# Performance work log

Hardware: AMD Instinct MI355X
Metric: run time of the kernel (lower is better)

## Reference

```python
import jax, jax.numpy as jnp
import numpy as np

K = 3        # kernel_size
EPS = 1e-4   # eps from __init__


def _conv_valid(x, w):
    # NHWC input, HWIO filter, VALID padding, stride 1
    return jax.lax.conv_general_dilated(
        x, w, window_strides=(1, 1), padding='VALID',
        dimension_numbers=('NHWC', 'HWIO', 'NHWC'))


def _backward_standardize_weight(grad_in, original_weights, gain, w_max_bitmap, eps):
    # Faithful translation of BackwardInjectWSConv2D.backward_standardize_weight
    kh, kw, cin, cout = original_weights.shape
    N = float(kh * kw * cin)                       # b*h*w in the TF code
    mu = jnp.mean(original_weights, axis=(0, 1, 2))
    xmu = original_weights - mu                    # [K,K,Cin,Cout]
    var = jnp.mean(jnp.square(xmu), axis=(0, 1, 2))
    mvar = N * var
    maxvar = jnp.maximum(mvar, eps)
    sqrtvar = jnp.sqrt(maxvar)
    ivar = 1.0 / sqrtvar
    givar = gain * ivar                            # [Cout]
    dgivar = jnp.sum(grad_in * xmu, axis=(0, 1, 2))
    divar = dgivar * gain
    dgain = dgivar * ivar
    dxmu1 = grad_in * givar
    dsqrtvar = (-1.0 / jnp.square(sqrtvar)) * divar
    dmaxvar = (0.5 / jnp.sqrt(maxvar)) * dsqrtvar
    dmvar = w_max_bitmap * dmaxvar
    dvar = N * dmvar
    dsq = (1.0 / N) * dvar                         # (1/N)*ones_like(grad_in)*dvar, broadcast
    dxmu2 = 2.0 * xmu * dsq
    dx1 = dxmu1 + dxmu2
    dmu = -jnp.sum(dx1, axis=(0, 1, 2))
    dx2 = (1.0 / N) * dmu                          # broadcast over [K,K,Cin]
    dx = dx1 + dx2
    return dx, dgain


def setup_inputs() -> dict:
    key = jax.random.key(0)
    ks = jax.random.split(key, 5)
    B, H, W, Cin, Cout = 64, 56, 56, 128, 128
    return {
        'grad_output': jax.random.normal(ks[0], (B, H, W, Cout), jnp.float32),
        'inputs': jax.random.normal(ks[1], (B, H, W, Cin), jnp.float32),
        'kernels': jax.random.normal(ks[2], (K, K, Cin, Cout), jnp.float32),
        'std_kernels': jax.random.normal(ks[3], (K, K, Cin, Cout), jnp.float32),
        'gain': jax.random.uniform(ks[4], (Cout,), jnp.float32),
        'w_max_bitmap': jnp.ones((Cout,), jnp.float32),
    }


def reference(grad_output, inputs, kernels, std_kernels, gain, w_max_bitmap):
    pad = (K - 1) // 2
    # ---- grad wrt input: full conv of grad_out with rot180(std_kernels), io swapped
    go_pad = jnp.pad(grad_output, ((0, 0), (pad, pad), (pad, pad), (0, 0)))
    w_rot = jnp.transpose(std_kernels[::-1, ::-1], (0, 1, 3, 2))   # [K,K,Cout,Cin]
    manual_grad_in = _conv_valid(go_pad, w_rot)                    # [B,H,W,Cin]
    # ---- grad wrt weight: treat Cin as batch, B as contraction channel
    in_pad = jnp.pad(inputs, ((0, 0), (pad, pad), (pad, pad), (0, 0)))
    fmt_inp = jnp.transpose(in_pad, (3, 1, 2, 0))                  # [Cin,H+2p,W+2p,B]
    fmt_wt = jnp.transpose(grad_output, (1, 2, 0, 3))              # [H,W,B,Cout]
    direct = _conv_valid(fmt_inp, fmt_wt)                          # [Cin,K,K,Cout]
    grad_wt_raw = jnp.transpose(direct, (1, 2, 0, 3))              # [K,K,Cin,Cout]
    # ---- weight-standardization backward chain
    manual_grad_wt, manual_grad_gain = _backward_standardize_weight(
        grad_wt_raw, kernels, gain, w_max_bitmap, EPS)
    # ---- bias grad
    manual_grad_bias = jnp.sum(grad_output, axis=(0, 1, 2))        # [Cout]
    return manual_grad_in, manual_grad_wt, manual_grad_bias, manual_grad_gain
```

## Files before the change

kernel.cpp:

```cpp
#include <hip/hip_runtime.h>
#include <hip/hip_bf16.h>

typedef __bf16 bf16x8 __attribute__((ext_vector_type(8)));
typedef __bf16 bf16x4 __attribute__((ext_vector_type(4)));
typedef float  f32x4  __attribute__((ext_vector_type(4)));
typedef unsigned int u32;

#define HW_   3136
#define NPIX  200704
#define GI_ELEMS 25690112

#define GOT_OFF   0u
#define RAW_OFF   51380224u
#define BIASA_OFF 51970048u
#define STDKF_OFF 51970560u
#define GUARD_OFF 52265472u
#define ZB_OFF    52265728u
#define ZA_OFF    52272000u
#define X_OFF     52279168u

__device__ __forceinline__ f32x4 mfma16(bf16x8 a, bf16x8 b, f32x4 c){
  return __builtin_amdgcn_mfma_f32_16x16x32_bf16(a, b, c, 0, 0, 0);
}

__device__ __forceinline__ void async16(const void* g, __bf16* l){
  __builtin_amdgcn_global_load_lds(
      (const __attribute__((address_space(1))) void*)g,
      (__attribute__((address_space(3))) void*)l, 16, 0, 0);
}

__global__ __launch_bounds__(256) void k_prep(const float* __restrict__ s, __bf16* __restrict__ d){
  const int g = blockIdx.x*256 + threadIdx.x;
  const int l = g & 63;
  const int j = (g >> 6) & 7;
  const int kc = (g >> 9) & 3;
  const int tap = g >> 11;
  const int ci = j*16 + (l & 15);
  const int co0 = kc*32 + (l >> 4)*8;
  const float* src = s + ((size_t)(tap*128 + ci))*128 + co0;
  f32x4 x0 = *(const f32x4*)src;
  f32x4 x1 = *(const f32x4*)(src + 4);
  bf16x8 y;
  #pragma unroll
  for (int e=0;e<4;e++){ y[e] = (__bf16)x0[e]; y[e+4] = (__bf16)x1[e]; }
  *(bf16x8*)(d + (size_t)g*8) = y;
}

__global__ __launch_bounds__(256) void k_goT(const float* __restrict__ go,
                                             __bf16* __restrict__ goT,
                                             __bf16* __restrict__ goB,
                                             float* __restrict__ biasA){
  __shared__ __bf16 T[64][130];
  __shared__ float biasS[128];
  const int t = threadIdx.x;
  const size_t p0 = (size_t)blockIdx.x*64;
  if (t < 128) biasS[t] = 0.f;
  __syncthreads();
  float bs[4] = {0.f,0.f,0.f,0.f};
  const int co0 = (t*4) & 127;
  #pragma unroll
  for (int i=0;i<8;i++){
    const int flat = (i*256+t)*4;
    const int px = flat >> 7, co = flat & 127;
    f32x4 x = *(const f32x4*)(go + p0*128 + flat);
    bf16x4 y;
    #pragma unroll
    for (int e=0;e<4;e++){ y[e] = (__bf16)x[e]; bs[e] += x[e]; }
    *(bf16x4*)&T[px][co] = y;
    *(bf16x4*)(goB + p0*128 + flat) = y;
  }
  #pragma unroll
  for (int e=0;e<4;e++) atomicAdd(&biasS[co0+e], bs[e]);
  __syncthreads();
  #pragma unroll
  for (int j=0;j<2;j++){
    const int task = j*256 + t;
    const int co = task >> 2, q = task & 3;
    bf16x8 v0, v1;
    #pragma unroll
    for (int k=0;k<8;k++) v0[k] = T[q*16+k][co];
    #pragma unroll
    for (int k=0;k<8;k++) v1[k] = T[q*16+8+k][co];
    __bf16* d = goT + (size_t)co*NPIX + p0 + q*16;
    *(bf16x8*)d = v0; *(bf16x8*)(d+8) = v1;
  }
  if (t < 128) atomicAdd(&biasA[t], biasS[t]);
}

__global__ __launch_bounds__(256) void k_inT(const float* __restrict__ inp,
                                             __bf16* __restrict__ inT){
  __shared__ __bf16 T[64][130];
  const int t = threadIdx.x;
  const size_t p0 = (size_t)blockIdx.x*64;

  if (blockIdx.x < 2304){
    const int g = blockIdx.x*256 + t;
    const int pair = g / 72, k = g - pair*72;
    __bf16* base = inT + (size_t)pair*3712;
    int off;
    if (k < 8)       off = k*8;
    else if (k < 16) off = 57*64 + (k-8)*8;
    else             off = (k-15)*64 + 56;
    bf16x8 z = {};
    *(bf16x8*)(base + off) = z;
  }

  #pragma unroll
  for (int i=0;i<8;i++){
    const int flat = (i*256+t)*4;
    const int px = flat >> 7, ci = flat & 127;
    f32x4 x = *(const f32x4*)(inp + p0*128 + flat);
    bf16x4 y;
    #pragma unroll
    for (int e=0;e<4;e++) y[e] = (__bf16)x[e];
    *(bf16x4*)&T[px][ci] = y;
  }
  __syncthreads();
  #pragma unroll
  for (int j=0;j<4;j++){
    const int task = j*256 + t;
    const int ci = task >> 3, ch = task & 7;
    const int p = (int)p0 + ch*8;
    const int b = p / HW_; const int r = p - b*HW_;
    const int h = r / 56;  const int w = r - h*56;
    bf16x8 v;
    #pragma unroll
    for (int k=0;k<8;k++) v[k] = T[ch*8+k][ci];
    *(bf16x8*)(inT + (((size_t)(ci*64+b))*58 + (h+1))*64 + w) = v;
  }
}

__global__ __launch_bounds__(256, 1) void k_gradin9(const __bf16* __restrict__ goB,
                                                    const __bf16* __restrict__ stdkF,
                                                    const __bf16* __restrict__ zsrc,
                                                    float* __restrict__ out){
  __shared__ char LDS[44544];
  const int t = threadIdx.x;
  const int wv = t >> 6, l = t & 63, lr = l & 15, lg = l >> 4;
  const int b = blockIdx.x, h0 = blockIdx.y*4;
  const int j0 = (wv & 1)*4;
  const int pxg = (wv >> 1)*112;

  int sb[7];
  #pragma unroll
  for (int tile=0; tile<7; ++tile){
    const int p = pxg + tile*16 + lr;
    const int ro = p / 56; const int w = p - ro*56;
    sb[tile] = (ro + 2)*58 + (w + 2);
  }

  f32x4 acc[7][4];
  #pragma unroll
  for (int i=0;i<7;i++){
    #pragma unroll
    for (int j=0;j<4;j++){
      #pragma unroll
      for (int r=0;r<4;r++) acc[i][j][r] = 0.f;
    }
  }

  for (int c=0; c<2; ++c){
    #pragma unroll
    for (int it=0; it<11; ++it){
      const int qb = it*256 + wv*64;
      const u32 q = (u32)(qb + l);
      if (q < 2784u){
        const u32 r = q / 464u;
        const u32 rem = q - r*464u;
        const u32 wp = rem >> 3;
        const u32 cl = rem & 7u;
        const int h = h0 - 1 + (int)r;
        const u32 s = r*58u + wp;
        const u32 csrc = cl ^ (s & 7u);
        const bool valid = (h >= 0) & (h < 56) & (wp >= 1u) & (wp <= 56u);
        const __bf16* src = valid
          ? goB + ((size_t)((b*HW_) + h*56 + ((int)wp - 1))*128 + c*64 + csrc*8)
          : zsrc;
        async16(src, (__bf16*)(LDS + qb*16));
      }
    }
    __syncthreads();

    for (int tap=0; tap<9; ++tap){
      const int u = tap/3;
      const int soff = u*58 + (tap - u*3);
      #pragma unroll
      for (int kc=0; kc<2; ++kc){
        const int kcg = c*2 + kc;
        bf16x8 Bf[4];
        #pragma unroll
        for (int j=0;j<4;++j)
          Bf[j] = *(const bf16x8*)(stdkF + ((size_t)(((tap*4 + kcg)*8 + j0 + j)*64 + l))*8);
        bf16x8 Af[7];
        #pragma unroll
        for (int tile=0;tile<7;++tile){
          const int s = sb[tile] - soff;
          const int byte = (s << 7) | (((kc*4 + lg) ^ (s & 7)) << 4);
          Af[tile] = *(const bf16x8*)(LDS + byte);
        }
        #pragma unroll
        for (int tile=0;tile<7;++tile){
          #pragma unroll
          for (int j=0;j<4;++j)
            acc[tile][j] = mfma16(Af[tile], Bf[j], acc[tile][j]);
        }
      }
    }
    __syncthreads();
  }

  float* o = out + ((size_t)b*HW_ + (size_t)h0*56 + pxg)*128;
  #pragma unroll
  for (int tile=0;tile<7;++tile){
    #pragma unroll
    for (int j=0;j<4;++j){
      #pragma unroll
      for (int r=0;r<4;++r)
        o[(size_t)(tile*16 + 4*lg + r)*128 + (j0 + j)*16 + lr] = acc[tile][j][r];
    }
  }
}

#define KSTEP9(ks)                                                             \
{                                                                              \
  const int pl = (ks)*32 + lg*8;                                               \
  const int q  = (ks)*4 + lg;                                                  \
  const int hl = q / 7;                                                        \
  const int w0 = pl - hl*56;                                                   \
  const int plc = ((ks)==3 && lg==3) ? 112 : pl;                               \
  bf16x8 b0 = *(const bf16x8*)&Bb[(wco + lr)*120 + plc];                       \
  bf16x8 b1 = *(const bf16x8*)&Bb[(wco + 16 + lr)*120 + plc];                  \
  const __bf16* abase = &Ab[lr*264 + hl*64 + w0];                              \
  _Pragma("unroll")                                                            \
  for (int u=0; u<3; ++u){                                                     \
    const __bf16* ap = abase + u*64;                                           \
    union { bf16x8 v; u32 d[4]; } vp, va, vn, a0, a2;                          \
    vp.v = *(const bf16x8*)(ap - 8);                                           \
    va.v = *(const bf16x8*)ap;                                                 \
    vn.v = *(const bf16x8*)(ap + 8);                                           \
    if ((ks)==3 && lg >= 2){                                                   \
      vp.d[0]=0u; vp.d[1]=0u; vp.d[2]=0u; vp.d[3]=0u;                          \
      va.d[0]=0u; va.d[1]=0u; va.d[2]=0u; va.d[3]=0u;                          \
      vn.d[0]=0u; vn.d[1]=0u; vn.d[2]=0u; vn.d[3]=0u;                          \
    }                                                                          \
    a0.d[0] = (va.d[0] << 16) | (vp.d[3] >> 16);                               \
    a0.d[1] = (va.d[1] << 16) | (va.d[0] >> 16);                               \
    a0.d[2] = (va.d[2] << 16) | (va.d[1] >> 16);                               \
    a0.d[3] = (va.d[3] << 16) | (va.d[2] >> 16);                               \
    a2.d[0] = (va.d[0] >> 16) | (va.d[1] << 16);                               \
    a2.d[1] = (va.d[1] >> 16) | (va.d[2] << 16);                               \
    a2.d[2] = (va.d[2] >> 16) | (va.d[3] << 16);                               \
    a2.d[3] = (va.d[3] >> 16) | (vn.d[0] << 16);                               \
    acc[u*3+0][0] = mfma16(a0.v, b0, acc[u*3+0][0]);                           \
    acc[u*3+0][1] = mfma16(a0.v, b1, acc[u*3+0][1]);                           \
    acc[u*3+1][0] = mfma16(va.v, b0, acc[u*3+1][0]);                           \
    acc[u*3+1][1] = mfma16(va.v, b1, acc[u*3+1][1]);                           \
    acc[u*3+2][0] = mfma16(a2.v, b0, acc[u*3+2][0]);                           \
    acc[u*3+2][1] = mfma16(a2.v, b1, acc[u*3+2][1]);                           \
  }                                                                            \
}

__global__ __launch_bounds__(256, 2) void k_gradwt9(const char* __restrict__ ws,
                                                    float* __restrict__ raw){
  __shared__ __bf16 LDS[39208];
  const int t = threadIdx.x;
  const int w = t >> 6, l = t & 63, lr = l & 15, lg = l >> 4;
  const int b = blockIdx.x, ci0 = blockIdx.y*16;
  const int wco = w*32;

  if (t < 40){
    const int idx = (t < 8) ? (30720 + t) : ((t < 24) ? (34952 + t - 8) : (39192 + t - 24));
    LDS[idx] = (__bf16)0.f;
  }

  u32 boff[8];
  #pragma unroll
  for (int i=0;i<8;i++){
    const int chunk = i*256 + t;
    if (chunk < 1920){
      const int co = chunk / 15, part = chunk - co*15;
      boff[i] = (part < 14)
        ? (GOT_OFF + (u32)(co*NPIX + b*HW_ + part*8)*2u)
        : ZB_OFF;
    } else boff[i] = ZB_OFF;
  }
  u32 aoff[3];
  #pragma unroll
  for (int i=0;i<3;i++){
    const int chunk = i*256 + t;
    if (chunk < 528){
      const int ci = chunk / 33, r = chunk - ci*33;
      aoff[i] = (r < 32)
        ? (X_OFF + (u32)((((ci0+ci)*64 + b)*58 + (r>>3))*64 + (r&7)*8)*2u)
        : ZA_OFF;
    } else aoff[i] = ZA_OFF;
  }

  f32x4 acc[9][2];
  #pragma unroll
  for (int tp=0;tp<9;tp++){
    #pragma unroll
    for (int j=0;j<2;j++){
      #pragma unroll
      for (int r=0;r<4;r++) acc[tp][j][r] = 0.f;
    }
  }

  #pragma unroll
  for (int i=0;i<8;i++){
    const int chunk = i*256 + t;
    if (chunk < 1920){ async16(ws + boff[i], LDS + chunk*8); boff[i] += 224u; }
  }
  #pragma unroll
  for (int i=0;i<3;i++){
    const int chunk = i*256 + t;
    if (chunk < 528){ async16(ws + aoff[i], LDS + 30728 + chunk*8); aoff[i] += 256u; }
  }
  __syncthreads();

  for (int c=0; c<28; ++c){
    const int cur = c & 1;
    if (c < 27){
      __bf16* dB = LDS + ((cur ^ 1) ? 15360 : 0);
      __bf16* dA = LDS + ((cur ^ 1) ? 34968 : 30728);
      #pragma unroll
      for (int i=0;i<8;i++){
        const int chunk = i*256 + t;
        if (chunk < 1920){ async16(ws + boff[i], dB + chunk*8); boff[i] += 224u; }
      }
      #pragma unroll
      for (int i=0;i<3;i++){
        const int chunk = i*256 + t;
        if (chunk < 528){ async16(ws + aoff[i], dA + chunk*8); aoff[i] += 256u; }
      }
    }
    const __bf16* Bb = LDS + (cur ? 15360 : 0);
    const __bf16* Ab = LDS + (cur ? 34968 : 30728);
    KSTEP9(0) KSTEP9(1) KSTEP9(2) KSTEP9(3)
    __syncthreads();
  }

  #pragma unroll
  for (int tp=0;tp<9;tp++){
    #pragma unroll
    for (int j=0;j<2;j++){
      #pragma unroll
      for (int r=0;r<4;r++)
        atomicAdd(&raw[(size_t)(tp*128 + ci0 + 4*lg + r)*128 + wco + j*16 + lr],
                  acc[tp][j][r]);
    }
  }
}

__global__ __launch_bounds__(128) void k_std(const float* __restrict__ raw,
      const float* __restrict__ kern, const float* __restrict__ gain,
      const float* __restrict__ bmap, const float* __restrict__ biasA,
      float* __restrict__ out_wt, float* __restrict__ out_bias, float* __restrict__ out_gain){
  const int co = blockIdx.x, t = threadIdx.x;
  float kv[9], gv[9];
  float s1=0.f, s2=0.f, sg=0.f, sgk=0.f;
  #pragma unroll
  for (int i=0;i<9;i++){
    const int m = t + i*128;
    const float k_ = kern[(size_t)m*128 + co];
    const float g_ = raw [(size_t)m*128 + co];
    kv[i]=k_; gv[i]=g_;
    s1 += k_; s2 += k_*k_; sg += g_; sgk += g_*k_;
  }
  __shared__ float red[4][128];
  red[0][t]=s1; red[1][t]=s2; red[2][t]=sg; red[3][t]=sgk;
  __syncthreads();
  for (int off=64; off>0; off>>=1){
    if (t < off){
      red[0][t]+=red[0][t+off]; red[1][t]+=red[1][t+off];
      red[2][t]+=red[2][t+off]; red[3][t]+=red[3][t+off];
    }
    __syncthreads();
  }
  const float N = 1152.f;
  const float S1=red[0][0], S2=red[1][0], Sg=red[2][0], Sgk=red[3][0];
  const float mu = S1/N;
  const float var = S2/N - mu*mu;
  const float mvar = N*var;
  const float maxvar = fmaxf(mvar, 1e-4f);
  const float sqrtvar = sqrtf(maxvar);
  const float ivar = 1.f/sqrtvar;
  const float g = gain[co];
  const float givar = g*ivar;
  const float dgivar = Sgk - mu*Sg;
  const float divar = dgivar*g;
  const float dsqrtvar = -divar/maxvar;
  const float dmaxvar = 0.5f*dsqrtvar/sqrtvar;
  const float dsq = bmap[co]*dmaxvar;
  const float dmu = -(givar*Sg + 2.f*dsq*(S1 - N*mu));
  const float dmuN = dmu*(1.f/N);
  #pragma unroll
  for (int i=0;i<9;i++){
    const int m = t + i*128;
    out_wt[(size_t)m*128 + co] = gv[i]*givar + 2.f*(kv[i]-mu)*dsq + dmuN;
  }
  if (t == 0){ out_gain[co] = dgivar*ivar; out_bias[co] = biasA[co]; }
}

extern "C" void kernel_launch(void* const* d_in, const int* in_sizes, int n_in,
                              void* d_out, int out_size, void* d_ws, size_t ws_size,
                              hipStream_t stream){
  const float* go   = (const float*)d_in[0];
  const float* inp  = (const float*)d_in[1];
  const float* kern = (const float*)d_in[2];
  const float* stdk = (const float*)d_in[3];
  const float* gain = (const float*)d_in[4];
  const float* bmap = (const float*)d_in[5];

  char* ws = (char*)d_ws;
  __bf16* goT   = (__bf16*)(ws + GOT_OFF);
  float*  raw   = (float*) (ws + RAW_OFF);
  float*  biasA = (float*) (ws + BIASA_OFF);
  __bf16* stdkF = (__bf16*)(ws + STDKF_OFF);
  char*   guard =           ws + GUARD_OFF;
  __bf16* goB   = (__bf16*)(ws + X_OFF);
  __bf16* inT   = (__bf16*)(ws + X_OFF);

  hipMemsetAsync(ws + RAW_OFF,   0, 589824 + 512, stream);
  hipMemsetAsync(ws + GUARD_OFF, 0, 256 + 6272 + 7168, stream);

  k_prep  <<<72, 256, 0, stream>>>(stdk, stdkF);
  k_goT   <<<3136, 256, 0, stream>>>(go, goT, goB, biasA);
  k_gradin9<<<dim3(64,14), 256, 0, stream>>>(goB, stdkF, (const __bf16*)guard, (float*)d_out);

  k_inT   <<<3136, 256, 0, stream>>>(inp, inT);
  k_gradwt9<<<dim3(64,8), 256, 0, stream>>>((const char*)ws, raw);

  float* out = (float*)d_out;
  k_std<<<128, 128, 0, stream>>>(raw, kern, gain, bmap, biasA,
                                 out + GI_ELEMS,
                                 out + GI_ELEMS + 147456,
                                 out + GI_ELEMS + 147456 + 128);
}
```

Measured before the change: 297.0 us.

## Fuse grad-input and grad-weight conv kernels into one heterogeneous launch

Moves the transposed input buffer to a separate workspace region so the goB buffer is no longer overwritten, which allows the grad-input and grad-weight convolutions to run in a single kernel. Blocks are interleaved 7:4 between the two jobs. The aim is to overlap the two GEMM-like phases, fill the GPU better and remove a launch boundary. The cost is a larger LDS allocation (78 KB, one block per CU) that also applies to the grad-weight blocks, which previously ran two per CU. The fused path is only taken when the workspace is large enough.

```diff
diff --git a/kernel.cpp b/kernel.cpp
--- a/kernel.cpp
+++ b/kernel.cpp
@@ -18,6 +18,8 @@
 #define ZB_OFF    52265728u
 #define ZA_OFF    52272000u
 #define X_OFF     52279168u
+#define X2_OFF    103659392u
+#define FUSED_WS  164476800u
 
 __device__ __forceinline__ f32x4 mfma16(bf16x8 a, bf16x8 b, f32x4 c){
   return __builtin_amdgcn_mfma_f32_16x16x32_bf16(a, b, c, 0, 0, 0);
@@ -130,14 +132,14 @@
   }
 }
 
-__global__ __launch_bounds__(256, 1) void k_gradin9(const __bf16* __restrict__ goB,
-                                                    const __bf16* __restrict__ stdkF,
-                                                    const __bf16* __restrict__ zsrc,
-                                                    float* __restrict__ out){
-  __shared__ char LDS[44544];
+__device__ __forceinline__ void dev_gradin(const __bf16* __restrict__ goB,
+                                           const __bf16* __restrict__ stdkF,
+                                           const __bf16* __restrict__ zsrc,
+                                           float* __restrict__ out,
+                                           char* LDS, const int b, const int hy){
   const int t = threadIdx.x;
   const int wv = t >> 6, l = t & 63, lr = l & 15, lg = l >> 4;
-  const int b = blockIdx.x, h0 = blockIdx.y*4;
+  const int h0 = hy*4;
   const int j0 = (wv & 1)*4;
   const int pxg = (wv >> 1)*112;
 
@@ -260,12 +262,13 @@
   }                                                                            \
 }
 
-__global__ __launch_bounds__(256, 2) void k_gradwt9(const char* __restrict__ ws,
-                                                    float* __restrict__ raw){
-  __shared__ __bf16 LDS[39208];
+__device__ __forceinline__ void dev_gradwt(const char* __restrict__ ws,
+                                           float* __restrict__ raw,
+                                           __bf16* LDS, const int b, const int ciy,
+                                           const u32 inTo){
   const int t = threadIdx.x;
   const int w = t >> 6, l = t & 63, lr = l & 15, lg = l >> 4;
-  const int b = blockIdx.x, ci0 = blockIdx.y*16;
+  const int ci0 = ciy*16;
   const int wco = w*32;
 
   if (t < 40){
@@ -291,7 +294,7 @@
     if (chunk < 528){
       const int ci = chunk / 33, r = chunk - ci*33;
       aoff[i] = (r < 32)
-        ? (X_OFF + (u32)((((ci0+ci)*64 + b)*58 + (r>>3))*64 + (r&7)*8)*2u)
+        ? (inTo + (u32)((((ci0+ci)*64 + b)*58 + (r>>3))*64 + (r&7)*8)*2u)
         : ZA_OFF;
     } else aoff[i] = ZA_OFF;
   }
@@ -349,6 +352,37 @@
         atomicAdd(&raw[(size_t)(tp*128 + ci0 + 4*lg + r)*128 + wco + j*16 + lr],
                   acc[tp][j][r]);
     }
+  }
+}
+
+__global__ __launch_bounds__(256, 1) void k_gradin9(const __bf16* __restrict__ goB,
+                                                    const __bf16* __restrict__ stdkF,
+                                                    const __bf16* __restrict__ zsrc,
+                                                    float* __restrict__ out){
+  __shared__ __align__(16) char LDS[44544];
+  dev_gradin(goB, stdkF, zsrc, out, LDS, blockIdx.x, blockIdx.y);
+}
+
+__global__ __launch_bounds__(256, 2) void k_gradwt9(const char* __restrict__ ws,
+                                                    float* __restrict__ raw, u32 inTo){
+  __shared__ __bf16 LDS[39208];
+  dev_gradwt(ws, raw, LDS, blockIdx.x, blockIdx.y, inTo);
+}
+
+__global__ __launch_bounds__(256, 1) void k_both(const char* __restrict__ ws,
+                                                 const __bf16* __restrict__ stdkF,
+                                                 const __bf16* __restrict__ zsrc,
+                                                 float* __restrict__ gin_out,
+                                                 float* __restrict__ raw, u32 inTo){
+  __shared__ __align__(16) char LDS[78416];
+  const int gid = blockIdx.x;
+  const int G = gid / 11, k = gid - G*11;
+  if (k < 7){
+    const int gi = G*7 + k;
+    dev_gradin((const __bf16*)(ws + X_OFF), stdkF, zsrc, gin_out, LDS, gi & 63, gi >> 6);
+  } else {
+    const int gw = G*4 + (k - 7);
+    dev_gradwt(ws, raw, (__bf16*)LDS, gw & 63, gw >> 6, inTo);
   }
 }
 
@@ -419,19 +453,28 @@
   __bf16* stdkF = (__bf16*)(ws + STDKF_OFF);
   char*   guard =           ws + GUARD_OFF;
   __bf16* goB   = (__bf16*)(ws + X_OFF);
-  __bf16* inT   = (__bf16*)(ws + X_OFF);
+
+  const bool fused = (ws_size >= (size_t)FUSED_WS);
+  const u32 inTo = fused ? X2_OFF : X_OFF;
+  __bf16* inT = (__bf16*)(ws + inTo);
 
   hipMemsetAsync(ws + RAW_OFF,   0, 589824 + 512, stream);
   hipMemsetAsync(ws + GUARD_OFF, 0, 256 + 6272 + 7168, stream);
 
-  k_prep  <<<72, 256, 0, stream>>>(stdk, stdkF);
-  k_goT   <<<3136, 256, 0, stream>>>(go, goT, goB, biasA);
-  k_gradin9<<<dim3(64,14), 256, 0, stream>>>(goB, stdkF, (const __bf16*)guard, (float*)d_out);
-
-  k_inT   <<<3136, 256, 0, stream>>>(inp, inT);
-  k_gradwt9<<<dim3(64,8), 256, 0, stream>>>((const char*)ws, raw);
+  k_prep<<<72, 256, 0, stream>>>(stdk, stdkF);
+  k_goT <<<3136, 256, 0, stream>>>(go, goT, goB, biasA);
 
   float* out = (float*)d_out;
+  if (fused){
+    k_inT <<<3136, 256, 0, stream>>>(inp, inT);
+    k_both<<<1408, 256, 0, stream>>>((const char*)ws, stdkF, (const __bf16*)guard,
+                                     out, raw, inTo);
+  } else {
+    k_gradin9<<<dim3(64,14), 256, 0, stream>>>(goB, stdkF, (const __bf16*)guard, out);
+    k_inT <<<3136, 256, 0, stream>>>(inp, inT);
+    k_gradwt9<<<dim3(64,8), 256, 0, stream>>>((const char*)ws, raw, inTo);
+  }
+
   k_std<<<128, 128, 0, stream>>>(raw, kern, gain, bmap, biasA,
                                  out + GI_ELEMS,
                                  out + GI_ELEMS + 147456,
```

Result: slower. 313.1 us (+5.4%).
